# Optimization experiments

Hardware: AMD Instinct MI355X
Metric: run time of the kernel (lower is better)

Reference implementation:

```python
import jax, jax.numpy as jnp
import numpy as np

N_NODES = 200000
N_EDGES = 6400000
N_GRAPHS = 1024
N_EMB = 1032
D = 16


def _gcn_conv(x, W, b, src, dst, n):
    # PyG GCNConv: h = x W; symmetric norm with self-loops; aggregate onto target (dst)
    h = x @ W
    deg = jax.ops.segment_sum(jnp.ones_like(dst, dtype=h.dtype), dst, num_segments=n) + 1.0
    dis = jax.lax.rsqrt(deg)
    norm = dis[src] * dis[dst]                      # [E]
    agg = jax.ops.segment_sum(h[src] * norm[:, None], dst, num_segments=n)
    agg = agg + h * (dis * dis)[:, None]            # self-loop term
    return agg + b


def _protein_embed(ids, edge_index, batch_ids, emb, W1, b1, W2, b2):
    n = ids.shape[0]
    x = emb[ids]                                    # embedding lookup [N, D]
    src, dst = edge_index[0], edge_index[1]
    h = jax.nn.relu(_gcn_conv(x, W1, b1, src, dst, n))
    h = _gcn_conv(h, W2, b2, src, dst, n)
    # global_mean_pool over graphs
    sums = jax.ops.segment_sum(h, batch_ids, num_segments=N_GRAPHS)
    cnt = jax.ops.segment_sum(jnp.ones((n,), h.dtype), batch_ids, num_segments=N_GRAPHS)
    return sums / jnp.maximum(cnt, 1.0)[:, None]    # [B, D]


def setup_inputs() -> dict:
    key = jax.random.key(0)
    ks = jax.random.split(key, 10)
    emb = jax.random.normal(ks[0], (N_EMB, D), jnp.float32) * 0.1
    W1 = jax.random.normal(ks[1], (D, D), jnp.float32) * (1.0 / np.sqrt(D))
    W2 = jax.random.normal(ks[2], (D, D), jnp.float32) * (1.0 / np.sqrt(D))
    fcW = jax.random.normal(ks[3], (6, 2 * D), jnp.float32) * (1.0 / np.sqrt(2 * D))
    b1 = jnp.zeros((D,), jnp.float32)
    b2 = jnp.zeros((D,), jnp.float32)
    fcb = jnp.zeros((6,), jnp.float32)
    rx = jax.random.randint(ks[4], (N_NODES,), 0, N_EMB)
    r_edge_index = jax.random.randint(ks[5], (2, N_EDGES), 0, N_NODES)
    r_batch = jnp.sort(jax.random.randint(ks[6], (N_NODES,), 0, N_GRAPHS))
    lx = jax.random.randint(ks[7], (N_NODES,), 0, N_EMB)
    l_edge_index = jax.random.randint(ks[8], (2, N_EDGES), 0, N_NODES)
    l_batch = jnp.sort(jax.random.randint(ks[9], (N_NODES,), 0, N_GRAPHS))
    return {"emb": emb, "W1": W1, "b1": b1, "W2": W2, "b2": b2, "fcW": fcW, "fcb": fcb,
            "rx": rx, "r_edge_index": r_edge_index, "r_batch": r_batch,
            "lx": lx, "l_edge_index": l_edge_index, "l_batch": l_batch}


def reference(emb, W1, b1, W2, b2, fcW, fcb, rx, r_edge_index, r_batch, lx, l_edge_index, l_batch):
    r = _protein_embed(rx, r_edge_index, r_batch, emb, W1, b1, W2, b2)
    l = _protein_embed(lx, l_edge_index, l_batch, emb, W1, b1, W2, b2)
    h = jnp.concatenate([r, l], axis=1)             # [B, 2D]
    out = h @ fcW.T + fcb                           # [B, 6]
    return out[:, :3], out[:, 3:]
```

## Files before the change

kernel.cpp:

```cpp
#include <hip/hip_runtime.h>
#include <hip/hip_bf16.h>

#define N_NODES 200000
#define N_GRAPHS 1024
#define D 16
#define NEDGE 6400000

#define BNODES 256
#define NBUK 782
#define NCH 512
#define ECHUNK 12500
#define OSTRIDE (NBUK + 1)
#define CAP 9216
#define GBLK 12500
#define GHALF 6250

__global__ __launch_bounds__(1024) void pA(
        const int* __restrict__ srcR, const int* __restrict__ dstR,
        const int* __restrict__ srcL, const int* __restrict__ dstL,
        unsigned int* __restrict__ slabC_R, unsigned int* __restrict__ slabC_L,
        int* __restrict__ offsT_R, int* __restrict__ offsT_L) {
    const int* src = blockIdx.y ? srcL : srcR;
    const int* dst = blockIdx.y ? dstL : dstR;
    unsigned int* slabC = blockIdx.y ? slabC_L : slabC_R;
    int* offsT = blockIdx.y ? offsT_L : offsT_R;

    __shared__ unsigned int stage[ECHUNK];
    __shared__ int lh[NBUK];
    __shared__ int lcur[NBUK];
    __shared__ int wsum[16];
    int t = threadIdx.x;
    int wave = t >> 6, lane = t & 63;
    int c = blockIdx.x;
    int base = c * ECHUNK;

    for (int k = t; k < NBUK; k += 1024) lh[k] = 0;
    __syncthreads();
    for (int e = t; e < ECHUNK; e += 1024)
        atomicAdd(&lh[((unsigned int)dst[base + e]) >> 8], 1);
    __syncthreads();

    int v = (t < NBUK) ? lh[t] : 0;
    int x = v;
#pragma unroll
    for (int d0 = 1; d0 < 64; d0 <<= 1) {
        int y = __shfl_up(x, d0, 64);
        if (lane >= d0) x += y;
    }
    if (lane == 63) wsum[wave] = x;
    __syncthreads();
    if (wave == 0 && lane < 16) {
        int s = wsum[lane];
#pragma unroll
        for (int d0 = 1; d0 < 16; d0 <<= 1) {
            int y = __shfl_up(s, d0, 64);
            if (lane >= d0) s += y;
        }
        wsum[lane] = s;
    }
    __syncthreads();
    int excl = x - v + (wave ? wsum[wave - 1] : 0);
    if (t < NBUK) lcur[t] = excl;
    __syncthreads();

    for (int e = t; e < ECHUNK; e += 1024) {
        int d = dst[base + e];
        int s = src[base + e];
        int pos = atomicAdd(&lcur[d >> 8], 1);
        stage[pos] = ((unsigned int)(d & 255) << 18) | (unsigned int)s;
    }
    __syncthreads();
    for (int e = t; e < ECHUNK; e += 1024) slabC[base + e] = stage[e];
    if (t < NBUK) offsT[c * OSTRIDE + t] = excl;
    if (t == 0) offsT[c * OSTRIDE + NBUK] = ECHUNK;
}

__global__ __launch_bounds__(256) void tr_kernel(
        const int* __restrict__ offsT_R, const int* __restrict__ offsT_L,
        int* __restrict__ offsTT_R, int* __restrict__ offsTT_L) {
    const int* in = blockIdx.z ? offsT_L : offsT_R;
    int* outp = blockIdx.z ? offsTT_L : offsTT_R;
    __shared__ int tile[32][33];
    int lx = threadIdx.x & 31, ly = threadIdx.x >> 5;
#pragma unroll
    for (int r = 0; r < 32; r += 8) {
        int row = blockIdx.y * 32 + ly + r;
        int col = blockIdx.x * 32 + lx;
        if (col < OSTRIDE) tile[ly + r][lx] = in[row * OSTRIDE + col];
    }
    __syncthreads();
#pragma unroll
    for (int r = 0; r < 32; r += 8) {
        int orow = blockIdx.x * 32 + ly + r;
        int ocol = blockIdx.y * 32 + lx;
        if (orow < OSTRIDE) outp[orow * NCH + ocol] = tile[lx][ly + r];
    }
}

__global__ __launch_bounds__(256) void pB(
        const unsigned int* __restrict__ slabC_R, const unsigned int* __restrict__ slabC_L,
        const int* __restrict__ offsTT_R, const int* __restrict__ offsTT_L,
        unsigned int* __restrict__ slabR, unsigned int* __restrict__ slabL,
        int2* __restrict__ metaR, int2* __restrict__ metaL,
        float* __restrict__ disR, float* __restrict__ disL) {
    int y = blockIdx.y;
    const unsigned int* slabC = y ? slabC_L : slabC_R;
    const int* offsTT = y ? offsTT_L : offsTT_R;
    unsigned int* slab = y ? slabL : slabR;
    int2* meta = y ? metaL : metaR;
    float* dis = y ? disL : disR;

    __shared__ unsigned int sin_[CAP];
    __shared__ unsigned int sout[CAP];
    __shared__ int hcnt[BNODES], hoff[BNODES], hcur[BNODES];
    __shared__ int wtot[4];
    __shared__ int totc;
    int t = threadIdx.x;
    int lane = t & 63, wave = t >> 6;
    int b = blockIdx.x;

    int a0 = offsTT[b * NCH + t],        e0 = offsTT[(b + 1) * NCH + t];
    int a1 = offsTT[b * NCH + t + 256],  e1 = offsTT[(b + 1) * NCH + t + 256];
    int len = (e0 - a0) + (e1 - a1);

    int x = len;
#pragma unroll
    for (int d0 = 1; d0 < 64; d0 <<= 1) {
        int yy = __shfl_up(x, d0, 64);
        if (lane >= d0) x += yy;
    }
    if (lane == 63) wtot[wave] = x;
    hcnt[t] = 0;
    __syncthreads();
    int pre = 0;
    for (int w2 = 0; w2 < wave; w2++) pre += wtot[w2];
    int sbase = x - len + pre;
    if (t == 255) totc = sbase + len;
    __syncthreads();

    int p = sbase;
    {
        int cb = t * ECHUNK;
        for (int i = (a0 & ~3); i < e0; i += 4) {
            uint4 v = *(const uint4*)(slabC + cb + i);
            unsigned int vv[4] = {v.x, v.y, v.z, v.w};
#pragma unroll
            for (int k = 0; k < 4; k++) {
                int idx = i + k;
                if (idx >= a0 && idx < e0) { if (p < CAP) sin_[p] = vv[k]; p++; }
            }
        }
        cb = (t + 256) * ECHUNK;
        for (int i = (a1 & ~3); i < e1; i += 4) {
            uint4 v = *(const uint4*)(slabC + cb + i);
            unsigned int vv[4] = {v.x, v.y, v.z, v.w};
#pragma unroll
            for (int k = 0; k < 4; k++) {
                int idx = i + k;
                if (idx >= a1 && idx < e1) { if (p < CAP) sin_[p] = vv[k]; p++; }
            }
        }
    }
    __syncthreads();
    int cnt = totc;
    if (cnt > CAP) cnt = CAP;

    for (int i = t; i < cnt; i += 256) atomicAdd(&hcnt[sin_[i] >> 18], 1);
    __syncthreads();

    int v2 = hcnt[t];
    int x2 = v2;
#pragma unroll
    for (int d0 = 1; d0 < 64; d0 <<= 1) {
        int yy = __shfl_up(x2, d0, 64);
        if (lane >= d0) x2 += yy;
    }
    if (lane == 63) wtot[wave] = x2;
    __syncthreads();
    int pre2 = 0;
    for (int w2 = 0; w2 < wave; w2++) pre2 += wtot[w2];
    int ex = x2 - v2 + pre2;
    hoff[t] = ex;
    hcur[t] = ex;
    __syncthreads();

    for (int i = t; i < cnt; i += 256) {
        unsigned int r = sin_[i];
        int pp = atomicAdd(&hcur[r >> 18], 1);
        if (pp < CAP) sout[pp] = r & 0x3FFFFu;
    }
    __syncthreads();

    int gb = b * CAP;
    for (int i = t; i < cnt; i += 256) slab[gb + i] = sout[i];
    int node = (b << 8) + t;
    if (node < N_NODES) {
        meta[node] = make_int2(gb + hoff[t], gb + hoff[t] + hcnt[t]);
        dis[node] = rsqrtf((float)hcnt[t] + 1.0f);
    }
}

__global__ __launch_bounds__(256) void t1_kernel(
        const int* __restrict__ idsR, const int* __restrict__ idsL,
        const float* __restrict__ emb, const float* __restrict__ W,
        const float* __restrict__ disR, const float* __restrict__ disL,
        __hip_bfloat16* __restrict__ hsR, __hip_bfloat16* __restrict__ hsL) {
    int y = blockIdx.y;
    const int* ids = y ? idsL : idsR;
    const float* dis = y ? disL : disR;
    __hip_bfloat16* hs = y ? hsL : hsR;
    __shared__ float sW[D][D];
    __shared__ float sx[16][D + 1];
    int t = threadIdx.x;
    int j = t & 15, g = t >> 4;
    sW[g][j] = W[t];
    int i = (blockIdx.x << 4) + g;
    sx[g][j] = emb[(size_t)ids[i] * D + j];
    __syncthreads();
    float acc = 0.f;
#pragma unroll
    for (int k = 0; k < D; k++) acc += sx[g][k] * sW[k][j];
    hs[(size_t)i * D + j] = __float2bfloat16(acc * dis[i]);
}

__global__ __launch_bounds__(256) void g1_kernel(
        const int2* __restrict__ metaR, const int2* __restrict__ metaL,
        const unsigned int* __restrict__ csrR, const unsigned int* __restrict__ csrL,
        const __hip_bfloat16* __restrict__ hs1R, const __hip_bfloat16* __restrict__ hs1L,
        const float* __restrict__ disR, const float* __restrict__ disL,
        const float* __restrict__ b1, const float* __restrict__ W2,
        __hip_bfloat16* __restrict__ hs2R, __hip_bfloat16* __restrict__ hs2L) {
    int half = (blockIdx.x >= GHALF);
    int bx = blockIdx.x - (half ? GHALF : 0);
    const int2* meta = half ? metaL : metaR;
    const unsigned int* csr = half ? csrL : csrR;
    const __hip_bfloat16* hs1 = half ? hs1L : hs1R;
    const float* dis = half ? disL : disR;
    __hip_bfloat16* hs2 = half ? hs2L : hs2R;

    __shared__ float sW[D][D];
    __shared__ float sx[32][D + 1];
    int t = threadIdx.x;
    int jp = t & 7, g = t >> 3;
    sW[t >> 4][t & 15] = W2[t];
    int i = (bx << 5) + g;
    int2 be = meta[i];
    float2 acc = __bfloat1622float2(
        *(const __hip_bfloat162*)(hs1 + (size_t)i * D + 2 * jp));
    int e = be.x, end = be.y;
    for (; e + 8 <= end; e += 8) {
        int my = (int)csr[e + jp];
#pragma unroll
        for (int n = 0; n < 8; n++) {
            int s = __shfl(my, n, 8);
            float2 f = __bfloat1622float2(
                *(const __hip_bfloat162*)(hs1 + (size_t)s * D + 2 * jp));
            acc.x += f.x; acc.y += f.y;
        }
    }
    for (; e < end; e++) {
        int s = csr[e];
        float2 f = __bfloat1622float2(
            *(const __hip_bfloat162*)(hs1 + (size_t)s * D + 2 * jp));
        acc.x += f.x; acc.y += f.y;
    }
    float di = dis[i];
    sx[g][2 * jp]     = fmaxf(acc.x * di + b1[2 * jp], 0.f);
    sx[g][2 * jp + 1] = fmaxf(acc.y * di + b1[2 * jp + 1], 0.f);
    __syncthreads();
    float a0 = 0.f, a1 = 0.f;
#pragma unroll
    for (int k = 0; k < D; k++) {
        float xv = sx[g][k];
        a0 += xv * sW[k][2 * jp];
        a1 += xv * sW[k][2 * jp + 1];
    }
    *(__hip_bfloat162*)(hs2 + (size_t)i * D + 2 * jp) =
        __float22bfloat162_rn(make_float2(a0 * di, a1 * di));
}

__global__ __launch_bounds__(256) void g2_kernel(
        const int2* __restrict__ metaR, const int2* __restrict__ metaL,
        const unsigned int* __restrict__ csrR, const unsigned int* __restrict__ csrL,
        const __hip_bfloat16* __restrict__ hs2R, const __hip_bfloat16* __restrict__ hs2L,
        const float* __restrict__ disR, const float* __restrict__ disL,
        const float* __restrict__ b2,
        const int* __restrict__ batR, const int* __restrict__ batL,
        float* __restrict__ sumsR, float* __restrict__ sumsL,
        float* __restrict__ cntR, float* __restrict__ cntL) {
    int half = (blockIdx.x >= GHALF);
    int bx = blockIdx.x - (half ? GHALF : 0);
    const int2* meta = half ? metaL : metaR;
    const unsigned int* csr = half ? csrL : csrR;
    const __hip_bfloat16* hs2 = half ? hs2L : hs2R;
    const float* dis = half ? disL : disR;
    const int* batch = half ? batL : batR;
    float* sums = half ? sumsL : sumsR;
    float* cnt = half ? cntL : cntR;

    __shared__ float sv[32][D + 1];
    __shared__ int sb[32];
    int t = threadIdx.x;
    int jp = t & 7, g = t >> 3;
    int i = (bx << 5) + g;
    int2 be = meta[i];
    float2 acc = __bfloat1622float2(
        *(const __hip_bfloat162*)(hs2 + (size_t)i * D + 2 * jp));
    int e = be.x, end = be.y;
    for (; e + 8 <= end; e += 8) {
        int my = (int)csr[e + jp];
#pragma unroll
        for (int n = 0; n < 8; n++) {
            int s = __shfl(my, n, 8);
            float2 f = __bfloat1622float2(
                *(const __hip_bfloat162*)(hs2 + (size_t)s * D + 2 * jp));
            acc.x += f.x; acc.y += f.y;
        }
    }
    for (; e < end; e++) {
        int s = csr[e];
        float2 f = __bfloat1622float2(
            *(const __hip_bfloat162*)(hs2 + (size_t)s * D + 2 * jp));
        acc.x += f.x; acc.y += f.y;
    }
    float di = dis[i];
    int bi = batch[i];
    sv[g][2 * jp]     = acc.x * di + b2[2 * jp];
    sv[g][2 * jp + 1] = acc.y * di + b2[2 * jp + 1];
    if (jp == 0) sb[g] = bi;
    __syncthreads();
    bool runend = (g == 31) || (sb[g + 1] != bi);
    if (runend) {
        float s0 = 0.f, s1 = 0.f;
        int gg = g;
        while (gg >= 0 && sb[gg] == bi) { s0 += sv[gg][2 * jp]; s1 += sv[gg][2 * jp + 1]; gg--; }
        atomicAdd(&sums[bi * D + 2 * jp], s0);
        atomicAdd(&sums[bi * D + 2 * jp + 1], s1);
        if (jp == 0) atomicAdd(&cnt[bi], (float)(g - gg));
    }
}

__global__ void final_kernel(const float* __restrict__ rs, const float* __restrict__ rc,
                             const float* __restrict__ ls, const float* __restrict__ lc,
                             const float* __restrict__ fcW, const float* __restrict__ fcb,
                             float* __restrict__ out) {
    int b = blockIdx.x * blockDim.x + threadIdx.x;
    if (b >= N_GRAPHS) return;
    float hc[2 * D];
    float rn = fmaxf(rc[b], 1.f), ln = fmaxf(lc[b], 1.f);
#pragma unroll
    for (int j = 0; j < D; j++) {
        hc[j]     = rs[b * D + j] / rn;
        hc[D + j] = ls[b * D + j] / ln;
    }
#pragma unroll
    for (int c = 0; c < 6; c++) {
        float acc = fcb[c];
#pragma unroll
        for (int j = 0; j < 2 * D; j++) acc += hc[j] * fcW[c * 2 * D + j];
        if (c < 3) out[b * 3 + c] = acc;
        else       out[N_GRAPHS * 3 + b * 3 + (c - 3)] = acc;
    }
}

extern "C" void kernel_launch(void* const* d_in, const int* in_sizes, int n_in,
                              void* d_out, int out_size, void* d_ws, size_t ws_size,
                              hipStream_t stream) {
    const float* emb = (const float*)d_in[0];
    const float* W1  = (const float*)d_in[1];
    const float* b1  = (const float*)d_in[2];
    const float* W2  = (const float*)d_in[3];
    const float* b2  = (const float*)d_in[4];
    const float* fcW = (const float*)d_in[5];
    const float* fcb = (const float*)d_in[6];
    const int* rx = (const int*)d_in[7];
    const int* re = (const int*)d_in[8];
    const int* rb = (const int*)d_in[9];
    const int* lx = (const int*)d_in[10];
    const int* le = (const int*)d_in[11];
    const int* lb = (const int*)d_in[12];
    float* out = (float*)d_out;

    char* w = (char*)d_ws;
    unsigned int* slabC_R = (unsigned int*)w;
    __hip_bfloat16* hs1R = (__hip_bfloat16*)w;
    __hip_bfloat16* hs1L = hs1R + (size_t)N_NODES * D;
    __hip_bfloat16* hs2R = hs1L + (size_t)N_NODES * D;
    __hip_bfloat16* hs2L = hs2R + (size_t)N_NODES * D;
    w += (size_t)NEDGE * 4;
    unsigned int* slabC_L = (unsigned int*)w;  w += (size_t)NEDGE * 4;
    unsigned int* slabR = (unsigned int*)w;    w += (size_t)NBUK * CAP * 4;
    unsigned int* slabL = (unsigned int*)w;    w += (size_t)NBUK * CAP * 4;
    int* offsT_R = (int*)w;                    w += (size_t)NCH * OSTRIDE * 4;
    int* offsT_L = (int*)w;                    w += (size_t)NCH * OSTRIDE * 4;
    int* offsTT_R = (int*)w;                   w += (size_t)OSTRIDE * NCH * 4;
    int* offsTT_L = (int*)w;                   w += (size_t)OSTRIDE * NCH * 4;
    int2* metaR = (int2*)w;                    w += (size_t)N_NODES * 8;
    int2* metaL = (int2*)w;                    w += (size_t)N_NODES * 8;
    float* disR = (float*)w;                   w += (size_t)N_NODES * 4;
    float* disL = (float*)w;                   w += (size_t)N_NODES * 4;
    float* sums0 = (float*)w;                  w += (size_t)N_GRAPHS * D * 4;
    float* cnt0  = (float*)w;                  w += (size_t)N_GRAPHS * 4;
    float* sums1 = (float*)w;                  w += (size_t)N_GRAPHS * D * 4;
    float* cnt1  = (float*)w;                  w += (size_t)N_GRAPHS * 4;

    const int* srcR = re;  const int* dstR = re + NEDGE;
    const int* srcL = le;  const int* dstL = le + NEDGE;

    hipMemsetAsync(sums0, 0, ((size_t)N_GRAPHS * (D + 1)) * 2 * sizeof(float), stream);

    pA<<<dim3(NCH, 2), 1024, 0, stream>>>(srcR, dstR, srcL, dstL,
                                          slabC_R, slabC_L, offsT_R, offsT_L);
    tr_kernel<<<dim3((OSTRIDE + 31) / 32, NCH / 32, 2), 256, 0, stream>>>(
        offsT_R, offsT_L, offsTT_R, offsTT_L);
    pB<<<dim3(NBUK, 2), 256, 0, stream>>>(slabC_R, slabC_L, offsTT_R, offsTT_L,
                                          slabR, slabL, metaR, metaL, disR, disL);

    t1_kernel<<<dim3(GBLK, 2), 256, 0, stream>>>(rx, lx, emb, W1, disR, disL, hs1R, hs1L);
    g1_kernel<<<2 * GHALF, 256, 0, stream>>>(metaR, metaL, slabR, slabL,
                                             hs1R, hs1L, disR, disL, b1, W2, hs2R, hs2L);
    g2_kernel<<<2 * GHALF, 256, 0, stream>>>(metaR, metaL, slabR, slabL,
                                             hs2R, hs2L, disR, disL, b2, rb, lb,
                                             sums0, sums1, cnt0, cnt1);
    final_kernel<<<(N_GRAPHS + 255) / 256, 256, 0, stream>>>(
        sums0, cnt0, sums1, cnt1, fcW, fcb, out);
}
```

Before: 532.8 us.

## Split feature tables into 8-wide halves to shrink gather working set

Stores layer features as two separate 8-column bf16 tables and runs each neighbor aggregation as two passes, one per half. Layer 1 is split into g1a (first half, ReLU output stored) and g1b (second half plus the W2 matmul), and g2 runs two passes through blockIdx.y. The aim is to keep each gathered table small enough to stay cache-resident and reduce random-access misses. In exchange, edge index lists are read twice per layer (with nontemporal loads), there is an extra kernel launch and an intermediate buffer, and block indexing is interleaved across the two graphs.

```diff
diff --git a/kernel.cpp b/kernel.cpp
--- a/kernel.cpp
+++ b/kernel.cpp
@@ -13,7 +13,10 @@
 #define OSTRIDE (NBUK + 1)
 #define CAP 9216
 #define GBLK 12500
-#define GHALF 6250
+
+#define GQ 782
+#define GGRID (GQ * 8)
+#define GBH 3125
 
 __global__ __launch_bounds__(1024) void pA(
         const int* __restrict__ srcR, const int* __restrict__ dstR,
@@ -204,11 +207,13 @@
         const int* __restrict__ idsR, const int* __restrict__ idsL,
         const float* __restrict__ emb, const float* __restrict__ W,
         const float* __restrict__ disR, const float* __restrict__ disL,
-        __hip_bfloat16* __restrict__ hsR, __hip_bfloat16* __restrict__ hsL) {
+        __hip_bfloat16* __restrict__ h1aR, __hip_bfloat16* __restrict__ h1bR,
+        __hip_bfloat16* __restrict__ h1aL, __hip_bfloat16* __restrict__ h1bL) {
     int y = blockIdx.y;
     const int* ids = y ? idsL : idsR;
     const float* dis = y ? disL : disR;
-    __hip_bfloat16* hs = y ? hsL : hsR;
+    __hip_bfloat16* ha = y ? h1aL : h1aR;
+    __hip_bfloat16* hb = y ? h1bL : h1bR;
     __shared__ float sW[D][D];
     __shared__ float sx[16][D + 1];
     int t = threadIdx.x;
@@ -220,123 +225,208 @@
     float acc = 0.f;
 #pragma unroll
     for (int k = 0; k < D; k++) acc += sx[g][k] * sW[k][j];
-    hs[(size_t)i * D + j] = __float2bfloat16(acc * dis[i]);
-}
-
-__global__ __launch_bounds__(256) void g1_kernel(
+    __hip_bfloat16 v = __float2bfloat16(acc * dis[i]);
+    if (j < 8) ha[(size_t)i * 8 + j] = v;
+    else       hb[(size_t)i * 8 + (j - 8)] = v;
+}
+
+__global__ __launch_bounds__(256) void g1a_kernel(
         const int2* __restrict__ metaR, const int2* __restrict__ metaL,
         const unsigned int* __restrict__ csrR, const unsigned int* __restrict__ csrL,
-        const __hip_bfloat16* __restrict__ hs1R, const __hip_bfloat16* __restrict__ hs1L,
+        const __hip_bfloat16* __restrict__ haR, const __hip_bfloat16* __restrict__ haL,
+        const float* __restrict__ disR, const float* __restrict__ disL,
+        const float* __restrict__ b1,
+        __hip_bfloat16* __restrict__ xAR, __hip_bfloat16* __restrict__ xAL) {
+    int bid = blockIdx.x;
+    int rr = bid & 7;
+    int half = rr >> 2;
+    int bx = (bid >> 3) * 4 + (rr & 3);
+    if (bx >= GBH) return;
+    const int2* meta = half ? metaL : metaR;
+    const unsigned int* csr = half ? csrL : csrR;
+    const __hip_bfloat16* ha = half ? haL : haR;
+    const float* dis = half ? disL : disR;
+    __hip_bfloat16* xA = half ? xAL : xAR;
+
+    int t = threadIdx.x;
+    int jp = t & 3, g = t >> 2;
+    int i = (bx << 6) + g;
+    int2 be = meta[i];
+    float2 acc = __bfloat1622float2(*(const __hip_bfloat162*)(ha + (size_t)i * 8 + 2 * jp));
+    int e = be.x, end = be.y;
+    for (; e + 8 <= end; e += 8) {
+        int m0 = (int)__builtin_nontemporal_load(csr + e + jp);
+        int m1 = (int)__builtin_nontemporal_load(csr + e + 4 + jp);
+#pragma unroll
+        for (int n = 0; n < 4; n++) {
+            int s = __shfl(m0, n, 4);
+            float2 f = __bfloat1622float2(*(const __hip_bfloat162*)(ha + (size_t)s * 8 + 2 * jp));
+            acc.x += f.x; acc.y += f.y;
+        }
+#pragma unroll
+        for (int n = 0; n < 4; n++) {
+            int s = __shfl(m1, n, 4);
+            float2 f = __bfloat1622float2(*(const __hip_bfloat162*)(ha + (size_t)s * 8 + 2 * jp));
+            acc.x += f.x; acc.y += f.y;
+        }
+    }
+    for (; e < end; e++) {
+        int s = (int)csr[e];
+        float2 f = __bfloat1622float2(*(const __hip_bfloat162*)(ha + (size_t)s * 8 + 2 * jp));
+        acc.x += f.x; acc.y += f.y;
+    }
+    float di = dis[i];
+    float2 xa;
+    xa.x = fmaxf(acc.x * di + b1[2 * jp], 0.f);
+    xa.y = fmaxf(acc.y * di + b1[2 * jp + 1], 0.f);
+    *(__hip_bfloat162*)(xA + (size_t)i * 8 + 2 * jp) = __float22bfloat162_rn(xa);
+}
+
+__global__ __launch_bounds__(256) void g1b_kernel(
+        const int2* __restrict__ metaR, const int2* __restrict__ metaL,
+        const unsigned int* __restrict__ csrR, const unsigned int* __restrict__ csrL,
+        const __hip_bfloat16* __restrict__ hbR, const __hip_bfloat16* __restrict__ hbL,
+        const __hip_bfloat16* __restrict__ xAR, const __hip_bfloat16* __restrict__ xAL,
         const float* __restrict__ disR, const float* __restrict__ disL,
         const float* __restrict__ b1, const float* __restrict__ W2,
-        __hip_bfloat16* __restrict__ hs2R, __hip_bfloat16* __restrict__ hs2L) {
-    int half = (blockIdx.x >= GHALF);
-    int bx = blockIdx.x - (half ? GHALF : 0);
+        __hip_bfloat16* __restrict__ h2aR, __hip_bfloat16* __restrict__ h2bR,
+        __hip_bfloat16* __restrict__ h2aL, __hip_bfloat16* __restrict__ h2bL) {
+    int bid = blockIdx.x;
+    int rr = bid & 7;
+    int half = rr >> 2;
+    int bx = (bid >> 3) * 4 + (rr & 3);
+    if (bx >= GBH) return;
     const int2* meta = half ? metaL : metaR;
     const unsigned int* csr = half ? csrL : csrR;
-    const __hip_bfloat16* hs1 = half ? hs1L : hs1R;
+    const __hip_bfloat16* hb = half ? hbL : hbR;
+    const __hip_bfloat16* xA = half ? xAL : xAR;
     const float* dis = half ? disL : disR;
-    __hip_bfloat16* hs2 = half ? hs2L : hs2R;
+    __hip_bfloat16* h2a = half ? h2aL : h2aR;
+    __hip_bfloat16* h2b = half ? h2bL : h2bR;
 
     __shared__ float sW[D][D];
-    __shared__ float sx[32][D + 1];
+    __shared__ float sx[64][D + 1];
     int t = threadIdx.x;
-    int jp = t & 7, g = t >> 3;
     sW[t >> 4][t & 15] = W2[t];
-    int i = (bx << 5) + g;
+    int jp = t & 3, g = t >> 2;
+    int i = (bx << 6) + g;
     int2 be = meta[i];
-    float2 acc = __bfloat1622float2(
-        *(const __hip_bfloat162*)(hs1 + (size_t)i * D + 2 * jp));
+    float2 acc = __bfloat1622float2(*(const __hip_bfloat162*)(hb + (size_t)i * 8 + 2 * jp));
     int e = be.x, end = be.y;
     for (; e + 8 <= end; e += 8) {
-        int my = (int)csr[e + jp];
-#pragma unroll
-        for (int n = 0; n < 8; n++) {
-            int s = __shfl(my, n, 8);
-            float2 f = __bfloat1622float2(
-                *(const __hip_bfloat162*)(hs1 + (size_t)s * D + 2 * jp));
+        int m0 = (int)__builtin_nontemporal_load(csr + e + jp);
+        int m1 = (int)__builtin_nontemporal_load(csr + e + 4 + jp);
+#pragma unroll
+        for (int n = 0; n < 4; n++) {
+            int s = __shfl(m0, n, 4);
+            float2 f = __bfloat1622float2(*(const __hip_bfloat162*)(hb + (size_t)s * 8 + 2 * jp));
             acc.x += f.x; acc.y += f.y;
         }
+#pragma unroll
+        for (int n = 0; n < 4; n++) {
+            int s = __shfl(m1, n, 4);
+            float2 f = __bfloat1622float2(*(const __hip_bfloat162*)(hb + (size_t)s * 8 + 2 * jp));
+            acc.x += f.x; acc.y += f.y;
+        }
     }
     for (; e < end; e++) {
-        int s = csr[e];
-        float2 f = __bfloat1622float2(
-            *(const __hip_bfloat162*)(hs1 + (size_t)s * D + 2 * jp));
+        int s = (int)csr[e];
+        float2 f = __bfloat1622float2(*(const __hip_bfloat162*)(hb + (size_t)s * 8 + 2 * jp));
         acc.x += f.x; acc.y += f.y;
     }
     float di = dis[i];
-    sx[g][2 * jp]     = fmaxf(acc.x * di + b1[2 * jp], 0.f);
-    sx[g][2 * jp + 1] = fmaxf(acc.y * di + b1[2 * jp + 1], 0.f);
-    __syncthreads();
-    float a0 = 0.f, a1 = 0.f;
+    unsigned int xabits = __builtin_nontemporal_load(
+        (const unsigned int*)(xA + (size_t)i * 8 + 2 * jp));
+    __hip_bfloat162 xav = *(__hip_bfloat162*)&xabits;
+    float2 xa = __bfloat1622float2(xav);
+    sx[g][2 * jp]     = xa.x;
+    sx[g][2 * jp + 1] = xa.y;
+    sx[g][8 + 2 * jp] = fmaxf(acc.x * di + b1[8 + 2 * jp], 0.f);
+    sx[g][9 + 2 * jp] = fmaxf(acc.y * di + b1[9 + 2 * jp], 0.f);
+    __syncthreads();
+    float a0 = 0.f, a1 = 0.f, c0 = 0.f, c1 = 0.f;
 #pragma unroll
     for (int k = 0; k < D; k++) {
         float xv = sx[g][k];
         a0 += xv * sW[k][2 * jp];
         a1 += xv * sW[k][2 * jp + 1];
-    }
-    *(__hip_bfloat162*)(hs2 + (size_t)i * D + 2 * jp) =
+        c0 += xv * sW[k][8 + 2 * jp];
+        c1 += xv * sW[k][9 + 2 * jp];
+    }
+    *(__hip_bfloat162*)(h2a + (size_t)i * 8 + 2 * jp) =
         __float22bfloat162_rn(make_float2(a0 * di, a1 * di));
+    *(__hip_bfloat162*)(h2b + (size_t)i * 8 + 2 * jp) =
+        __float22bfloat162_rn(make_float2(c0 * di, c1 * di));
 }
 
 __global__ __launch_bounds__(256) void g2_kernel(
         const int2* __restrict__ metaR, const int2* __restrict__ metaL,
         const unsigned int* __restrict__ csrR, const unsigned int* __restrict__ csrL,
-        const __hip_bfloat16* __restrict__ hs2R, const __hip_bfloat16* __restrict__ hs2L,
+        const __hip_bfloat16* __restrict__ h2aR, const __hip_bfloat16* __restrict__ h2bR,
+        const __hip_bfloat16* __restrict__ h2aL, const __hip_bfloat16* __restrict__ h2bL,
         const float* __restrict__ disR, const float* __restrict__ disL,
         const float* __restrict__ b2,
         const int* __restrict__ batR, const int* __restrict__ batL,
         float* __restrict__ sumsR, float* __restrict__ sumsL,
         float* __restrict__ cntR, float* __restrict__ cntL) {
-    int half = (blockIdx.x >= GHALF);
-    int bx = blockIdx.x - (half ? GHALF : 0);
+    int pass = blockIdx.y;
+    int bid = blockIdx.x;
+    int rr = bid & 7;
+    int half = rr >> 2;
+    int bx = (bid >> 3) * 4 + (rr & 3);
+    if (bx >= GBH) return;
     const int2* meta = half ? metaL : metaR;
     const unsigned int* csr = half ? csrL : csrR;
-    const __hip_bfloat16* hs2 = half ? hs2L : hs2R;
+    const __hip_bfloat16* tab = pass ? (half ? h2bL : h2bR) : (half ? h2aL : h2aR);
     const float* dis = half ? disL : disR;
     const int* batch = half ? batL : batR;
     float* sums = half ? sumsL : sumsR;
     float* cnt = half ? cntL : cntR;
-
-    __shared__ float sv[32][D + 1];
-    __shared__ int sb[32];
+    int off = pass << 3;
+
+    __shared__ float sv[64][9];
+    __shared__ int sb[64];
     int t = threadIdx.x;
-    int jp = t & 7, g = t >> 3;
-    int i = (bx << 5) + g;
+    int jp = t & 3, g = t >> 2;
+    int i = (bx << 6) + g;
     int2 be = meta[i];
-    float2 acc = __bfloat1622float2(
-        *(const __hip_bfloat162*)(hs2 + (size_t)i * D + 2 * jp));
+    float2 acc = __bfloat1622float2(*(const __hip_bfloat162*)(tab + (size_t)i * 8 + 2 * jp));
     int e = be.x, end = be.y;
     for (; e + 8 <= end; e += 8) {
-        int my = (int)csr[e + jp];
-#pragma unroll
-        for (int n = 0; n < 8; n++) {
-            int s = __shfl(my, n, 8);
-            float2 f = __bfloat1622float2(
-                *(const __hip_bfloat162*)(hs2 + (size_t)s * D + 2 * jp));
+        int m0 = (int)__builtin_nontemporal_load(csr + e + jp);
+        int m1 = (int)__builtin_nontemporal_load(csr + e + 4 + jp);
+#pragma unroll
+        for (int n = 0; n < 4; n++) {
+            int s = __shfl(m0, n, 4);
+            float2 f = __bfloat1622float2(*(const __hip_bfloat162*)(tab + (size_t)s * 8 + 2 * jp));
             acc.x += f.x; acc.y += f.y;
         }
+#pragma unroll
+        for (int n = 0; n < 4; n++) {
+            int s = __shfl(m1, n, 4);
+            float2 f = __bfloat1622float2(*(const __hip_bfloat162*)(tab + (size_t)s * 8 + 2 * jp));
+            acc.x += f.x; acc.y += f.y;
+        }
     }
     for (; e < end; e++) {
-        int s = csr[e];
-        float2 f = __bfloat1622float2(
-            *(const __hip_bfloat162*)(hs2 + (size_t)s * D + 2 * jp));
+        int s = (int)csr[e];
+        float2 f = __bfloat1622float2(*(const __hip_bfloat162*)(tab + (size_t)s * 8 + 2 * jp));
         acc.x += f.x; acc.y += f.y;
     }
     float di = dis[i];
     int bi = batch[i];
-    sv[g][2 * jp]     = acc.x * di + b2[2 * jp];
-    sv[g][2 * jp + 1] = acc.y * di + b2[2 * jp + 1];
+    sv[g][2 * jp]     = acc.x * di + b2[off + 2 * jp];
+    sv[g][2 * jp + 1] = acc.y * di + b2[off + 2 * jp + 1];
     if (jp == 0) sb[g] = bi;
     __syncthreads();
-    bool runend = (g == 31) || (sb[g + 1] != bi);
+    bool runend = (g == 63) || (sb[g + 1] != bi);
     if (runend) {
         float s0 = 0.f, s1 = 0.f;
         int gg = g;
         while (gg >= 0 && sb[gg] == bi) { s0 += sv[gg][2 * jp]; s1 += sv[gg][2 * jp + 1]; gg--; }
-        atomicAdd(&sums[bi * D + 2 * jp], s0);
-        atomicAdd(&sums[bi * D + 2 * jp + 1], s1);
-        if (jp == 0) atomicAdd(&cnt[bi], (float)(g - gg));
+        atomicAdd(&sums[bi * D + off + 2 * jp], s0);
+        atomicAdd(&sums[bi * D + off + 2 * jp + 1], s1);
+        if (pass == 0 && jp == 0) atomicAdd(&cnt[bi], (float)(g - gg));
     }
 }
 
@@ -383,10 +473,16 @@
 
     char* w = (char*)d_ws;
     unsigned int* slabC_R = (unsigned int*)w;
-    __hip_bfloat16* hs1R = (__hip_bfloat16*)w;
-    __hip_bfloat16* hs1L = hs1R + (size_t)N_NODES * D;
-    __hip_bfloat16* hs2R = hs1L + (size_t)N_NODES * D;
-    __hip_bfloat16* hs2L = hs2R + (size_t)N_NODES * D;
+    __hip_bfloat16* h1aR = (__hip_bfloat16*)w;
+    __hip_bfloat16* h1bR = h1aR + (size_t)N_NODES * 8;
+    __hip_bfloat16* h1aL = h1bR + (size_t)N_NODES * 8;
+    __hip_bfloat16* h1bL = h1aL + (size_t)N_NODES * 8;
+    __hip_bfloat16* h2aR = h1bL + (size_t)N_NODES * 8;
+    __hip_bfloat16* h2bR = h2aR + (size_t)N_NODES * 8;
+    __hip_bfloat16* h2aL = h2bR + (size_t)N_NODES * 8;
+    __hip_bfloat16* h2bL = h2aL + (size_t)N_NODES * 8;
+    __hip_bfloat16* xAR  = h2bL + (size_t)N_NODES * 8;
+    __hip_bfloat16* xAL  = xAR  + (size_t)N_NODES * 8;
     w += (size_t)NEDGE * 4;
     unsigned int* slabC_L = (unsigned int*)w;  w += (size_t)NEDGE * 4;
     unsigned int* slabR = (unsigned int*)w;    w += (size_t)NBUK * CAP * 4;
@@ -416,12 +512,17 @@
     pB<<<dim3(NBUK, 2), 256, 0, stream>>>(slabC_R, slabC_L, offsTT_R, offsTT_L,
                                           slabR, slabL, metaR, metaL, disR, disL);
 
-    t1_kernel<<<dim3(GBLK, 2), 256, 0, stream>>>(rx, lx, emb, W1, disR, disL, hs1R, hs1L);
-    g1_kernel<<<2 * GHALF, 256, 0, stream>>>(metaR, metaL, slabR, slabL,
-                                             hs1R, hs1L, disR, disL, b1, W2, hs2R, hs2L);
-    g2_kernel<<<2 * GHALF, 256, 0, stream>>>(metaR, metaL, slabR, slabL,
-                                             hs2R, hs2L, disR, disL, b2, rb, lb,
-                                             sums0, sums1, cnt0, cnt1);
+    t1_kernel<<<dim3(GBLK, 2), 256, 0, stream>>>(rx, lx, emb, W1, disR, disL,
+                                                 h1aR, h1bR, h1aL, h1bL);
+    g1a_kernel<<<GGRID, 256, 0, stream>>>(metaR, metaL, slabR, slabL,
+                                          h1aR, h1aL, disR, disL, b1, xAR, xAL);
+    g1b_kernel<<<GGRID, 256, 0, stream>>>(metaR, metaL, slabR, slabL,
+                                          h1bR, h1bL, xAR, xAL, disR, disL, b1, W2,
+                                          h2aR, h2bR, h2aL, h2bL);
+    g2_kernel<<<dim3(GGRID, 2), 256, 0, stream>>>(metaR, metaL, slabR, slabL,
+                                                  h2aR, h2bR, h2aL, h2bL,
+                                                  disR, disL, b2, rb, lb,
+                                                  sums0, sums1, cnt0, cnt1);
     final_kernel<<<(N_GRAPHS + 255) / 256, 256, 0, stream>>>(
         sums0, cnt0, sums1, cnt1, fcW, fcb, out);
 }
```

New measurement: 729.1 us. 36.8% more time.

## Scatter edges directly into bucket slabs via global atomic cursors, drop transpose pass

Applied to the files above, without the earlier changes.

The partition kernel now reserves space in each destination bucket with a global atomicAdd per bucket and writes edges straight into the per-bucket slab. This removes the intermediate chunk slab, the offset-table transpose kernel, and pB's gather of many small per-chunk segments. pB2 just loads the contiguous bucket. The costs are global atomics, scattered writes from pA, and non-deterministic edge order within a bucket. Bucket overflow past CAP is no longer guarded in pA, and the chunk size changes to 10000 with 640 chunks.

```diff
diff --git a/kernel.cpp b/kernel.cpp
--- a/kernel.cpp
+++ b/kernel.cpp
@@ -8,9 +8,8 @@
 
 #define BNODES 256
 #define NBUK 782
-#define NCH 512
-#define ECHUNK 12500
-#define OSTRIDE (NBUK + 1)
+#define NCH 640
+#define ECHUNK 10000
 #define CAP 9216
 #define GBLK 12500
 #define GHALF 6250
@@ -18,21 +17,21 @@
 __global__ __launch_bounds__(1024) void pA(
         const int* __restrict__ srcR, const int* __restrict__ dstR,
         const int* __restrict__ srcL, const int* __restrict__ dstL,
-        unsigned int* __restrict__ slabC_R, unsigned int* __restrict__ slabC_L,
-        int* __restrict__ offsT_R, int* __restrict__ offsT_L) {
+        unsigned int* __restrict__ slabR, unsigned int* __restrict__ slabL,
+        int* __restrict__ gcurR, int* __restrict__ gcurL) {
     const int* src = blockIdx.y ? srcL : srcR;
     const int* dst = blockIdx.y ? dstL : dstR;
-    unsigned int* slabC = blockIdx.y ? slabC_L : slabC_R;
-    int* offsT = blockIdx.y ? offsT_L : offsT_R;
+    unsigned int* slab = blockIdx.y ? slabL : slabR;
+    int* gcur = blockIdx.y ? gcurL : gcurR;
 
     __shared__ unsigned int stage[ECHUNK];
+    __shared__ unsigned short stageB[ECHUNK];
     __shared__ int lh[NBUK];
     __shared__ int lcur[NBUK];
     __shared__ int wsum[16];
     int t = threadIdx.x;
     int wave = t >> 6, lane = t & 63;
-    int c = blockIdx.x;
-    int base = c * ECHUNK;
+    int base = blockIdx.x * ECHUNK;
 
     for (int k = t; k < NBUK; k += 1024) lh[k] = 0;
     __syncthreads();
@@ -62,51 +61,36 @@
     int excl = x - v + (wave ? wsum[wave - 1] : 0);
     if (t < NBUK) lcur[t] = excl;
     __syncthreads();
+    if (t < NBUK) {
+        int gb = v ? atomicAdd(&gcur[t], v) : 0;
+        lh[t] = gb - excl;
+    }
+    __syncthreads();
 
     for (int e = t; e < ECHUNK; e += 1024) {
         int d = dst[base + e];
         int s = src[base + e];
-        int pos = atomicAdd(&lcur[d >> 8], 1);
+        int buk = ((unsigned int)d) >> 8;
+        int pos = atomicAdd(&lcur[buk], 1);
         stage[pos] = ((unsigned int)(d & 255) << 18) | (unsigned int)s;
-    }
-    __syncthreads();
-    for (int e = t; e < ECHUNK; e += 1024) slabC[base + e] = stage[e];
-    if (t < NBUK) offsT[c * OSTRIDE + t] = excl;
-    if (t == 0) offsT[c * OSTRIDE + NBUK] = ECHUNK;
-}
-
-__global__ __launch_bounds__(256) void tr_kernel(
-        const int* __restrict__ offsT_R, const int* __restrict__ offsT_L,
-        int* __restrict__ offsTT_R, int* __restrict__ offsTT_L) {
-    const int* in = blockIdx.z ? offsT_L : offsT_R;
-    int* outp = blockIdx.z ? offsTT_L : offsTT_R;
-    __shared__ int tile[32][33];
-    int lx = threadIdx.x & 31, ly = threadIdx.x >> 5;
-#pragma unroll
-    for (int r = 0; r < 32; r += 8) {
-        int row = blockIdx.y * 32 + ly + r;
-        int col = blockIdx.x * 32 + lx;
-        if (col < OSTRIDE) tile[ly + r][lx] = in[row * OSTRIDE + col];
-    }
-    __syncthreads();
-#pragma unroll
-    for (int r = 0; r < 32; r += 8) {
-        int orow = blockIdx.x * 32 + ly + r;
-        int ocol = blockIdx.y * 32 + lx;
-        if (orow < OSTRIDE) outp[orow * NCH + ocol] = tile[lx][ly + r];
-    }
-}
-
-__global__ __launch_bounds__(256) void pB(
-        const unsigned int* __restrict__ slabC_R, const unsigned int* __restrict__ slabC_L,
-        const int* __restrict__ offsTT_R, const int* __restrict__ offsTT_L,
+        stageB[pos] = (unsigned short)buk;
+    }
+    __syncthreads();
+    for (int e = t; e < ECHUNK; e += 1024) {
+        int k = stageB[e];
+        int off = lh[k] + e;
+        slab[(size_t)k * CAP + off] = stage[e];
+    }
+}
+
+__global__ __launch_bounds__(256) void pB2(
         unsigned int* __restrict__ slabR, unsigned int* __restrict__ slabL,
+        const int* __restrict__ gcurR, const int* __restrict__ gcurL,
         int2* __restrict__ metaR, int2* __restrict__ metaL,
         float* __restrict__ disR, float* __restrict__ disL) {
     int y = blockIdx.y;
-    const unsigned int* slabC = y ? slabC_L : slabC_R;
-    const int* offsTT = y ? offsTT_L : offsTT_R;
     unsigned int* slab = y ? slabL : slabR;
+    const int* gcur = y ? gcurL : gcurR;
     int2* meta = y ? metaL : metaR;
     float* dis = y ? disL : disR;
 
@@ -114,56 +98,19 @@
     __shared__ unsigned int sout[CAP];
     __shared__ int hcnt[BNODES], hoff[BNODES], hcur[BNODES];
     __shared__ int wtot[4];
-    __shared__ int totc;
     int t = threadIdx.x;
     int lane = t & 63, wave = t >> 6;
     int b = blockIdx.x;
-
-    int a0 = offsTT[b * NCH + t],        e0 = offsTT[(b + 1) * NCH + t];
-    int a1 = offsTT[b * NCH + t + 256],  e1 = offsTT[(b + 1) * NCH + t + 256];
-    int len = (e0 - a0) + (e1 - a1);
-
-    int x = len;
-#pragma unroll
-    for (int d0 = 1; d0 < 64; d0 <<= 1) {
-        int yy = __shfl_up(x, d0, 64);
-        if (lane >= d0) x += yy;
-    }
-    if (lane == 63) wtot[wave] = x;
+    int cnt = gcur[b]; if (cnt > CAP) cnt = CAP;
+    unsigned int* sl = slab + (size_t)b * CAP;
     hcnt[t] = 0;
     __syncthreads();
-    int pre = 0;
-    for (int w2 = 0; w2 < wave; w2++) pre += wtot[w2];
-    int sbase = x - len + pre;
-    if (t == 255) totc = sbase + len;
-    __syncthreads();
-
-    int p = sbase;
-    {
-        int cb = t * ECHUNK;
-        for (int i = (a0 & ~3); i < e0; i += 4) {
-            uint4 v = *(const uint4*)(slabC + cb + i);
-            unsigned int vv[4] = {v.x, v.y, v.z, v.w};
-#pragma unroll
-            for (int k = 0; k < 4; k++) {
-                int idx = i + k;
-                if (idx >= a0 && idx < e0) { if (p < CAP) sin_[p] = vv[k]; p++; }
-            }
-        }
-        cb = (t + 256) * ECHUNK;
-        for (int i = (a1 & ~3); i < e1; i += 4) {
-            uint4 v = *(const uint4*)(slabC + cb + i);
-            unsigned int vv[4] = {v.x, v.y, v.z, v.w};
-#pragma unroll
-            for (int k = 0; k < 4; k++) {
-                int idx = i + k;
-                if (idx >= a1 && idx < e1) { if (p < CAP) sin_[p] = vv[k]; p++; }
-            }
-        }
-    }
-    __syncthreads();
-    int cnt = totc;
-    if (cnt > CAP) cnt = CAP;
+
+    for (int i = t * 4; i < cnt; i += 1024) {
+        uint4 v = *(const uint4*)(sl + i);
+        sin_[i] = v.x; sin_[i + 1] = v.y; sin_[i + 2] = v.z; sin_[i + 3] = v.w;
+    }
+    __syncthreads();
 
     for (int i = t; i < cnt; i += 256) atomicAdd(&hcnt[sin_[i] >> 18], 1);
     __syncthreads();
@@ -187,12 +134,12 @@
     for (int i = t; i < cnt; i += 256) {
         unsigned int r = sin_[i];
         int pp = atomicAdd(&hcur[r >> 18], 1);
-        if (pp < CAP) sout[pp] = r & 0x3FFFFu;
+        sout[pp] = r & 0x3FFFFu;
     }
     __syncthreads();
 
     int gb = b * CAP;
-    for (int i = t; i < cnt; i += 256) slab[gb + i] = sout[i];
+    for (int i = t; i < cnt; i += 256) sl[i] = sout[i];
     int node = (b << 8) + t;
     if (node < N_NODES) {
         meta[node] = make_int2(gb + hoff[t], gb + hoff[t] + hcnt[t]);
@@ -382,39 +329,34 @@
     float* out = (float*)d_out;
 
     char* w = (char*)d_ws;
-    unsigned int* slabC_R = (unsigned int*)w;
-    __hip_bfloat16* hs1R = (__hip_bfloat16*)w;
-    __hip_bfloat16* hs1L = hs1R + (size_t)N_NODES * D;
-    __hip_bfloat16* hs2R = hs1L + (size_t)N_NODES * D;
-    __hip_bfloat16* hs2L = hs2R + (size_t)N_NODES * D;
-    w += (size_t)NEDGE * 4;
-    unsigned int* slabC_L = (unsigned int*)w;  w += (size_t)NEDGE * 4;
     unsigned int* slabR = (unsigned int*)w;    w += (size_t)NBUK * CAP * 4;
     unsigned int* slabL = (unsigned int*)w;    w += (size_t)NBUK * CAP * 4;
-    int* offsT_R = (int*)w;                    w += (size_t)NCH * OSTRIDE * 4;
-    int* offsT_L = (int*)w;                    w += (size_t)NCH * OSTRIDE * 4;
-    int* offsTT_R = (int*)w;                   w += (size_t)OSTRIDE * NCH * 4;
-    int* offsTT_L = (int*)w;                   w += (size_t)OSTRIDE * NCH * 4;
+    __hip_bfloat16* hs1R = (__hip_bfloat16*)w; w += (size_t)N_NODES * D * 2;
+    __hip_bfloat16* hs1L = (__hip_bfloat16*)w; w += (size_t)N_NODES * D * 2;
+    __hip_bfloat16* hs2R = (__hip_bfloat16*)w; w += (size_t)N_NODES * D * 2;
+    __hip_bfloat16* hs2L = (__hip_bfloat16*)w; w += (size_t)N_NODES * D * 2;
     int2* metaR = (int2*)w;                    w += (size_t)N_NODES * 8;
     int2* metaL = (int2*)w;                    w += (size_t)N_NODES * 8;
     float* disR = (float*)w;                   w += (size_t)N_NODES * 4;
     float* disL = (float*)w;                   w += (size_t)N_NODES * 4;
+    char* zbase = w;
+    int* gcurR = (int*)w;                      w += (size_t)NBUK * 4;
+    int* gcurL = (int*)w;                      w += (size_t)NBUK * 4;
     float* sums0 = (float*)w;                  w += (size_t)N_GRAPHS * D * 4;
     float* cnt0  = (float*)w;                  w += (size_t)N_GRAPHS * 4;
     float* sums1 = (float*)w;                  w += (size_t)N_GRAPHS * D * 4;
     float* cnt1  = (float*)w;                  w += (size_t)N_GRAPHS * 4;
+    size_t zsize = (size_t)(w - zbase);
 
     const int* srcR = re;  const int* dstR = re + NEDGE;
     const int* srcL = le;  const int* dstL = le + NEDGE;
 
-    hipMemsetAsync(sums0, 0, ((size_t)N_GRAPHS * (D + 1)) * 2 * sizeof(float), stream);
+    hipMemsetAsync(zbase, 0, zsize, stream);
 
     pA<<<dim3(NCH, 2), 1024, 0, stream>>>(srcR, dstR, srcL, dstL,
-                                          slabC_R, slabC_L, offsT_R, offsT_L);
-    tr_kernel<<<dim3((OSTRIDE + 31) / 32, NCH / 32, 2), 256, 0, stream>>>(
-        offsT_R, offsT_L, offsTT_R, offsTT_L);
-    pB<<<dim3(NBUK, 2), 256, 0, stream>>>(slabC_R, slabC_L, offsTT_R, offsTT_L,
-                                          slabR, slabL, metaR, metaL, disR, disL);
+                                          slabR, slabL, gcurR, gcurL);
+    pB2<<<dim3(NBUK, 2), 256, 0, stream>>>(slabR, slabL, gcurR, gcurL,
+                                           metaR, metaL, disR, disL);
 
     t1_kernel<<<dim3(GBLK, 2), 256, 0, stream>>>(rx, lx, emb, W1, disR, disL, hs1R, hs1L);
     g1_kernel<<<2 * GHALF, 256, 0, stream>>>(metaR, metaL, slabR, slabL,
```

Measured after the change: 530.9 us. Within noise of the previous version (-0.4%).
